# Performance work log

Hardware: AMD Instinct MI355X
Metric: run time of the kernel (lower is better)

## Reference

```python
import jax, jax.numpy as jnp
import numpy as np

# MLA (multi-head latent attention) config
DIM = 1024
HEADS = 16
DIM_HEAD = DIM // HEADS          # 64
LATENT = DIM // 4                # 256, compressed KV latent dim
SCALE = DIM_HEAD ** -0.5


def setup_inputs() -> dict:
    key = jax.random.key(0)
    ks = jax.random.split(key, 8)
    B, S = 2, 2048
    init = lambda k, shape, fan_in: jax.random.normal(k, shape, jnp.float32) * (fan_in ** -0.5)
    return {
        "x":  jax.random.normal(ks[0], (B, S, DIM), jnp.float32),
        "Wq": init(ks[1], (DIM, DIM), DIM),
        "bq": jnp.zeros((DIM,), jnp.float32),
        "Wl": init(ks[2], (DIM, LATENT), DIM),      # down-projection to compressed KV latent
        "bl": jnp.zeros((LATENT,), jnp.float32),
        "Wk": init(ks[3], (LATENT, DIM), LATENT),   # latent -> per-head keys
        "bk": jnp.zeros((DIM,), jnp.float32),
        "Wv": init(ks[4], (LATENT, DIM), LATENT),   # latent -> per-head values
        "bv": jnp.zeros((DIM,), jnp.float32),
        "Wo": init(ks[5], (DIM, DIM), DIM),         # Attention.to_out
        "bo": jnp.zeros((DIM,), jnp.float32),
    }


def reference(x, Wq, bq, Wl, bl, Wk, bk, Wv, bv, Wo, bo):
    B, S, D = x.shape
    H, Dh = HEADS, DIM_HEAD
    # query projection
    q = (x @ Wq + bq).reshape(B, S, H, Dh)
    # compressed KV latent (this is what would be cached; kv_cache=None here)
    latent = x @ Wl + bl                              # [B, S, LATENT]
    k = (latent @ Wk + bk).reshape(B, S, H, Dh)
    v = (latent @ Wv + bv).reshape(B, S, H, Dh)
    # attention
    scores = jnp.einsum('bihd,bjhd->bhij', q, k) * SCALE   # [B, H, S, S]
    attn = jax.nn.softmax(scores, axis=-1)
    out = jnp.einsum('bhij,bjhd->bihd', attn, v).reshape(B, S, D)
    # dropout(p=0) is identity; output projection
    out = out @ Wo + bo
    return out
```

## Files before the change

kernel.cpp:

```cpp
#include <hip/hip_runtime.h>


typedef _Float16 half8  __attribute__((ext_vector_type(8)));
typedef _Float16 half4  __attribute__((ext_vector_type(4)));
typedef float    floatx4 __attribute__((ext_vector_type(4)));

__global__ __launch_bounds__(256) void prep(
    const float* __restrict__ x,
    const float* __restrict__ Wq, const float* __restrict__ Wl,
    const float* __restrict__ Wk, const float* __restrict__ Wv,
    const float* __restrict__ Wo,
    _Float16* __restrict__ xh,
    _Float16* __restrict__ Bt1, _Float16* __restrict__ Bt2,
    _Float16* __restrict__ Wot)
{
    const int t = threadIdx.x;
    if (blockIdx.z == 5) {
        size_t base = ((size_t)(blockIdx.y * 32 + blockIdx.x) * 256 + t) * 16;
#pragma unroll
        for (int it = 0; it < 4; ++it) {
            floatx4 v = *(const floatx4*)(x + base + it * 4);
            *(half4*)(xh + base + it * 4) = __builtin_convertvector(v, half4);
        }
        return;
    }
    const float* src; _Float16* dst; int K, N;
    switch (blockIdx.z) {
        case 0:  src = Wq; dst = Bt1;                 K = 1024; N = 1024; break;
        case 1:  src = Wl; dst = Bt1 + 1024 * 1024;   K = 1024; N = 256;  break;
        case 2:  src = Wk; dst = Bt2;                 K = 256;  N = 1024; break;
        case 3:  src = Wv; dst = Bt2 + 1024 * 256;    K = 256;  N = 1024; break;
        default: src = Wo; dst = Wot;                 K = 1024; N = 1024; break;
    }
    const int n0 = blockIdx.x * 32, k0 = blockIdx.y * 32;
    if (n0 >= N || k0 >= K) return;
    __shared__ _Float16 tile[32][33];
    const int tx = t & 31, ty = t >> 5;
#pragma unroll
    for (int i = 0; i < 4; ++i)
        tile[ty + 8 * i][tx] = (_Float16)src[(size_t)(k0 + ty + 8 * i) * N + n0 + tx];
    __syncthreads();
#pragma unroll
    for (int i = 0; i < 4; ++i)
        dst[(size_t)(n0 + ty + 8 * i) * K + k0 + tx] = tile[tx][ty + 8 * i];
}

template <int MODE>
__global__ __launch_bounds__(256) void gemm_fused(
    const _Float16* __restrict__ A, const _Float16* __restrict__ Bt,
    const float* __restrict__ bias0, const float* __restrict__ bias1,
    void* __restrict__ out0, void* __restrict__ out1,
    int N, int K)
{
    __shared__ _Float16 As[128 * 64];
    __shared__ _Float16 Bs[64 * 64];
    __shared__ _Float16 Tt[(MODE == 1) ? 64 * 136 : 1];
    const int t = threadIdx.x;
    const int lane = t & 63, w = t >> 6;
    const int quad = lane >> 4, low = lane & 15;
    const int row0 = blockIdx.y * 128, col0 = blockIdx.x * 64;
    const int wm = (w >> 1) * 64, wn = (w & 1) * 32;

    floatx4 acc[4][2];
    const floatx4 z4 = {0.f, 0.f, 0.f, 0.f};
#pragma unroll
    for (int i = 0; i < 4; ++i)
#pragma unroll
        for (int j = 0; j < 2; ++j) acc[i][j] = z4;

    const int srow8 = lane >> 3;
    const int sslot = lane & 7;
    const int fswz = (low & 7);

    for (int k0 = 0; k0 < K; k0 += 64) {
        __syncthreads();
#pragma unroll
        for (int c = 0; c < 4; ++c) {
            const int chunk = w * 4 + c;
            const int row = chunk * 8 + srow8;
            const int g = sslot ^ (row & 7);
            const _Float16* gp = A + (size_t)(row0 + row) * K + k0 + g * 8;
            __builtin_amdgcn_global_load_lds(
                (const __attribute__((address_space(1))) void*)gp,
                (__attribute__((address_space(3))) void*)(As + chunk * 512), 16, 0, 0);
        }
#pragma unroll
        for (int c = 0; c < 2; ++c) {
            const int chunk = w * 2 + c;
            const int row = chunk * 8 + srow8;
            const int g = sslot ^ (row & 7);
            const _Float16* gp = Bt + (size_t)(col0 + row) * K + k0 + g * 8;
            __builtin_amdgcn_global_load_lds(
                (const __attribute__((address_space(1))) void*)gp,
                (__attribute__((address_space(3))) void*)(Bs + chunk * 512), 16, 0, 0);
        }
        __syncthreads();

#pragma unroll
        for (int kk = 0; kk < 2; ++kk) {
            const int slot = ((4 * kk + quad) ^ fswz) << 3;
            half8 a[4], b[2];
#pragma unroll
            for (int i = 0; i < 4; ++i)
                a[i] = *(const half8*)(As + (wm + i * 16 + low) * 64 + slot);
#pragma unroll
            for (int j = 0; j < 2; ++j)
                b[j] = *(const half8*)(Bs + (wn + j * 16 + low) * 64 + slot);
#pragma unroll
            for (int i = 0; i < 4; ++i)
#pragma unroll
                for (int j = 0; j < 2; ++j)
                    acc[i][j] = __builtin_amdgcn_mfma_f32_16x16x32_f16(a[i], b[j], acc[i][j], 0, 0, 0);
        }
    }

    if (MODE == 1 && col0 >= 1024) {
        const int hh = (col0 - 1024) >> 6;
        const int bb = row0 >> 11;
        const int tok0 = row0 & 2047;
#pragma unroll
        for (int i = 0; i < 4; ++i)
#pragma unroll
            for (int j = 0; j < 2; ++j) {
                const int lc = wn + j * 16 + low;
                float bv = bias1[hh * 64 + lc];
                half4 ph;
#pragma unroll
                for (int r = 0; r < 4; ++r) ph[r] = (_Float16)(acc[i][j][r] + bv);
                *(half4*)(&Tt[lc * 136 + wm + i * 16 + quad * 4]) = ph;
            }
        __syncthreads();
        _Float16* vb = (_Float16*)out1 + ((size_t)(bb * 16 + hh) * 64) * 2048;
#pragma unroll
        for (int it = 0; it < 4; ++it) {
            const int e = t + 256 * it;
            const int d = e >> 4, tk = (e & 15) * 8;
            half8 val = *(const half8*)(&Tt[d * 136 + tk]);
            *(half8*)(vb + (size_t)d * 2048 + tok0 + tk) = val;
        }
        return;
    }

#pragma unroll
    for (int i = 0; i < 4; ++i) {
#pragma unroll
        for (int j = 0; j < 2; ++j) {
            const int col = col0 + wn + j * 16 + low;
            const int rbase = row0 + wm + i * 16 + quad * 4;
            if (MODE == 2) {
                const float bv = bias0[col];
#pragma unroll
                for (int r = 0; r < 4; ++r)
                    ((float*)out0)[(size_t)(rbase + r) * 1024 + col] = acc[i][j][r] + bv;
            } else if (col < 1024) {
                float bv = bias0[col];
#pragma unroll
                for (int r = 0; r < 4; ++r) {
                    float val = acc[i][j][r] + bv;
                    if (MODE == 0) val *= 0.125f;
                    ((_Float16*)out0)[(size_t)(rbase + r) * 1024 + col] = (_Float16)val;
                }
            } else {
                const int c2 = col - 1024;
                float bv = bias1[c2];
#pragma unroll
                for (int r = 0; r < 4; ++r)
                    ((_Float16*)out1)[(size_t)(rbase + r) * 256 + c2] =
                        (_Float16)(acc[i][j][r] + bv);
            }
        }
    }
}

__global__ __launch_bounds__(256, 4) void mla_attn(
    const _Float16* __restrict__ qp,
    const _Float16* __restrict__ kk,
    const _Float16* __restrict__ vt,
    _Float16* __restrict__ Op0, _Float16* __restrict__ Op1,
    float* __restrict__ lp)
{
    constexpr int S = 2048;
    __shared__ _Float16 Ks[64][76];
    __shared__ _Float16 Vs[64][76];
    __shared__ _Float16 Ps[128][76];

    const int t = threadIdx.x, lane = t & 63, w = t >> 6;
    const int quad = lane >> 4, low = lane & 15;
    const int q0 = blockIdx.x * 128;
    const int b = blockIdx.y >> 4, h = blockIdx.y & 15;
    const int split = blockIdx.z;

    half8 qf[2][2];
#pragma unroll
    for (int ni = 0; ni < 2; ++ni)
#pragma unroll
        for (int ks = 0; ks < 2; ++ks)
            qf[ni][ks] = *(const half8*)(qp +
                (size_t)(b * S + q0 + w * 32 + ni * 16 + low) * 1024 +
                h * 64 + ks * 32 + quad * 8);

    floatx4 oa[2][4], ls[2];
    const floatx4 z4 = {0.f, 0.f, 0.f, 0.f};
#pragma unroll
    for (int mi = 0; mi < 2; ++mi) {
        ls[mi] = z4;
#pragma unroll
        for (int nd = 0; nd < 4; ++nd) oa[mi][nd] = z4;
    }

    const _Float16* kbase = kk + (size_t)(b * S) * 1024 + h * 64;
    const _Float16* vbase = vt + (size_t)(b * 16 + h) * 64 * 2048;

    const int jbeg = split * 1024, jend = jbeg + 1024;
    for (int j0 = jbeg; j0 < jend; j0 += 64) {
        __syncthreads();
#pragma unroll
        for (int p = 0; p < 2; ++p) {
            int c = p * 256 + t;
            int r = c >> 3, o8 = (c & 7) * 8;
            *(half8*)(&Ks[r][o8]) = *(const half8*)(kbase + (size_t)(j0 + r) * 1024 + o8);
            *(half8*)(&Vs[r][o8]) = *(const half8*)(vbase + (size_t)r * 2048 + j0 + o8);
        }
        __syncthreads();

        floatx4 s[4][2];
        const floatx4 i4 = {-3.f, -3.f, -3.f, -3.f};
#pragma unroll
        for (int mj = 0; mj < 4; ++mj)
#pragma unroll
            for (int ni = 0; ni < 2; ++ni) s[mj][ni] = i4;
#pragma unroll
        for (int ks = 0; ks < 2; ++ks) {
            half8 af[4];
#pragma unroll
            for (int mj = 0; mj < 4; ++mj)
                af[mj] = *(const half8*)(&Ks[mj * 16 + low][ks * 32 + quad * 8]);
#pragma unroll
            for (int mj = 0; mj < 4; ++mj)
#pragma unroll
                for (int ni = 0; ni < 2; ++ni)
                    s[mj][ni] = __builtin_amdgcn_mfma_f32_16x16x32_f16(af[mj], qf[ni][ks], s[mj][ni], 0, 0, 0);
        }

#pragma unroll
        for (int mj = 0; mj < 4; ++mj)
#pragma unroll
            for (int ni = 0; ni < 2; ++ni) {
                floatx4 pv;
#pragma unroll
                for (int r = 0; r < 4; ++r) pv[r] = __expf(s[mj][ni][r]);
                ls[ni] += pv;
                half4 ph;
#pragma unroll
                for (int r = 0; r < 4; ++r) ph[r] = (_Float16)pv[r];
                *(half4*)(&Ps[w * 32 + ni * 16 + low][mj * 16 + quad * 4]) = ph;
            }

#pragma unroll
        for (int ks = 0; ks < 2; ++ks) {
            half8 pf[2], vf[4];
#pragma unroll
            for (int mi = 0; mi < 2; ++mi)
                pf[mi] = *(const half8*)(&Ps[w * 32 + mi * 16 + low][ks * 32 + quad * 8]);
#pragma unroll
            for (int nd = 0; nd < 4; ++nd)
                vf[nd] = *(const half8*)(&Vs[nd * 16 + low][ks * 32 + quad * 8]);
#pragma unroll
            for (int mi = 0; mi < 2; ++mi)
#pragma unroll
                for (int nd = 0; nd < 4; ++nd)
                    oa[mi][nd] = __builtin_amdgcn_mfma_f32_16x16x32_f16(pf[mi], vf[nd], oa[mi][nd], 0, 0, 0);
        }
    }

#pragma unroll
    for (int ni = 0; ni < 2; ++ni) {
        float l = ls[ni][0] + ls[ni][1] + ls[ni][2] + ls[ni][3];
        l += __shfl_xor(l, 16);
        l += __shfl_xor(l, 32);
        if (quad == 0)
            lp[split * 65536 + (b * 16 + h) * 2048 + q0 + w * 32 + ni * 16 + low] = l;
    }
    _Float16* op = split ? Op1 : Op0;
#pragma unroll
    for (int mi = 0; mi < 2; ++mi)
#pragma unroll
        for (int nd = 0; nd < 4; ++nd)
#pragma unroll
            for (int r = 0; r < 4; ++r)
                op[(size_t)(b * S + q0 + w * 32 + mi * 16 + quad * 4 + r) * 1024 +
                   h * 64 + nd * 16 + low] = (_Float16)oa[mi][nd][r];
}

__global__ __launch_bounds__(256) void attn_combine(
    const _Float16* __restrict__ O0, const _Float16* __restrict__ O1,
    const float* __restrict__ lp, _Float16* __restrict__ att)
{
    size_t idx = ((size_t)blockIdx.x * 256 + threadIdx.x) * 8;
    int row = (int)(idx >> 10), c = (int)(idx & 1023);
    int b = row >> 11, qq = row & 2047, h = c >> 6;
    int li = (b * 16 + h) * 2048 + qq;
    float inv = 1.f / (lp[li] + lp[65536 + li]);
    half8 a = *(const half8*)(O0 + idx);
    half8 bb = *(const half8*)(O1 + idx);
    half8 o;
#pragma unroll
    for (int r = 0; r < 8; ++r)
        o[r] = (_Float16)(((float)a[r] + (float)bb[r]) * inv);
    *(half8*)(att + idx) = o;
}

extern "C" void kernel_launch(void* const* d_in, const int* in_sizes, int n_in,
                              void* d_out, int out_size, void* d_ws, size_t ws_size,
                              hipStream_t stream) {
    const float* x  = (const float*)d_in[0];
    const float* Wq = (const float*)d_in[1];
    const float* bq = (const float*)d_in[2];
    const float* Wl = (const float*)d_in[3];
    const float* bl = (const float*)d_in[4];
    const float* Wk = (const float*)d_in[5];
    const float* bk = (const float*)d_in[6];
    const float* Wv = (const float*)d_in[7];
    const float* bv = (const float*)d_in[8];
    const float* Wo = (const float*)d_in[9];
    const float* bo = (const float*)d_in[10];
    float* out = (float*)d_out;

    _Float16* p   = (_Float16*)d_ws;
    _Float16* xh  = p; p += 4194304;
    _Float16* qh  = p; p += 4194304;
    _Float16* kh  = p; p += 4194304;
    _Float16* vtb = p; p += 4194304;
    _Float16* ah  = p; p += 4194304;
    _Float16* lat = p; p += 1048576;
    _Float16* Bt1 = p; p += 1310720;
    _Float16* Bt2 = p; p += 524288;
    _Float16* Wot = p; p += 1048576;

    prep<<<dim3(32, 32, 6), 256, 0, stream>>>(x, Wq, Wl, Wk, Wv, Wo, xh, Bt1, Bt2, Wot);

    gemm_fused<0><<<dim3(20, 32), 256, 0, stream>>>(
        xh, Bt1, bq, bl, qh, lat, 1280, 1024);
    gemm_fused<1><<<dim3(32, 32), 256, 0, stream>>>(
        lat, Bt2, bk, bv, kh, vtb, 2048, 256);
    mla_attn<<<dim3(16, 32, 2), 256, 0, stream>>>(qh, kh, vtb, ah, xh, (float*)lat);
    attn_combine<<<2048, 256, 0, stream>>>(ah, xh, (const float*)lat, kh);
    gemm_fused<2><<<dim3(16, 32), 256, 0, stream>>>(
        kh, Wot, bo, nullptr, out, nullptr, 1024, 1024);
}
```

Before: 211.7 us.

## Keep P in registers via 32x32 MFMA and permlane swap, swizzle K/V LDS

Rewrites the attention inner loop to use 32x32x16 MFMA tiles so the exponentiated score tile can be repacked into the A operand of the PV matmul with v_permlane32_swap instead of staging P through shared memory. The padded K/V/P shared buffers become unpadded K/V tiles with an XOR-and-rotate swizzle to avoid bank conflicts. The P buffer and its LDS round-trip are removed and the occupancy hint on launch bounds is dropped. In exchange the fragment layout mapping is more intricate and register pressure per wave changes.

```diff
diff --git a/kernel.cpp b/kernel.cpp
--- a/kernel.cpp
+++ b/kernel.cpp
@@ -4,6 +4,7 @@
 typedef _Float16 half8  __attribute__((ext_vector_type(8)));
 typedef _Float16 half4  __attribute__((ext_vector_type(4)));
 typedef float    floatx4 __attribute__((ext_vector_type(4)));
+typedef float    floatx16 __attribute__((ext_vector_type(16)));
 
 __global__ __launch_bounds__(256) void prep(
     const float* __restrict__ x,
@@ -172,7 +173,12 @@
     }
 }
 
-__global__ __launch_bounds__(256, 4) void mla_attn(
+__device__ __forceinline__ unsigned pk2(float a, float b) {
+    union { _Float16 h[2]; unsigned u; } x;
+    x.h[0] = (_Float16)a; x.h[1] = (_Float16)b; return x.u;
+}
+
+__global__ __launch_bounds__(256) void mla_attn(
     const _Float16* __restrict__ qp,
     const _Float16* __restrict__ kk,
     const _Float16* __restrict__ vt,
@@ -180,33 +186,28 @@
     float* __restrict__ lp)
 {
     constexpr int S = 2048;
-    __shared__ _Float16 Ks[64][76];
-    __shared__ _Float16 Vs[64][76];
-    __shared__ _Float16 Ps[128][76];
+    __shared__ _Float16 Ks[64 * 64];
+    __shared__ _Float16 Vs[64 * 64];
 
     const int t = threadIdx.x, lane = t & 63, w = t >> 6;
-    const int quad = lane >> 4, low = lane & 15;
+    const int l31 = lane & 31, hi = lane >> 5;
+    const int rho = l31 & 7, sig = l31 >> 3;
     const int q0 = blockIdx.x * 128;
     const int b = blockIdx.y >> 4, h = blockIdx.y & 15;
     const int split = blockIdx.z;
 
-    half8 qf[2][2];
-#pragma unroll
-    for (int ni = 0; ni < 2; ++ni)
-#pragma unroll
-        for (int ks = 0; ks < 2; ++ks)
-            qf[ni][ks] = *(const half8*)(qp +
-                (size_t)(b * S + q0 + w * 32 + ni * 16 + low) * 1024 +
-                h * 64 + ks * 32 + quad * 8);
-
-    floatx4 oa[2][4], ls[2];
-    const floatx4 z4 = {0.f, 0.f, 0.f, 0.f};
-#pragma unroll
-    for (int mi = 0; mi < 2; ++mi) {
-        ls[mi] = z4;
-#pragma unroll
-        for (int nd = 0; nd < 4; ++nd) oa[mi][nd] = z4;
-    }
+    half8 qf[4];
+#pragma unroll
+    for (int ks = 0; ks < 4; ++ks)
+        qf[ks] = *(const half8*)(qp +
+            (size_t)(b * S + q0 + w * 32 + l31) * 1024 + h * 64 + ks * 16 + hi * 8);
+
+    floatx16 oa[2];
+#pragma unroll
+    for (int nd = 0; nd < 2; ++nd)
+#pragma unroll
+        for (int r = 0; r < 16; ++r) oa[nd][r] = 0.f;
+    float ls = 0.f;
 
     const _Float16* kbase = kk + (size_t)(b * S) * 1024 + h * 64;
     const _Float16* vbase = vt + (size_t)(b * 16 + h) * 64 * 2048;
@@ -216,80 +217,81 @@
         __syncthreads();
 #pragma unroll
         for (int p = 0; p < 2; ++p) {
-            int c = p * 256 + t;
-            int r = c >> 3, o8 = (c & 7) * 8;
-            *(half8*)(&Ks[r][o8]) = *(const half8*)(kbase + (size_t)(j0 + r) * 1024 + o8);
-            *(half8*)(&Vs[r][o8]) = *(const half8*)(vbase + (size_t)r * 2048 + j0 + o8);
-        }
-        __syncthreads();
-
-        floatx4 s[4][2];
-        const floatx4 i4 = {-3.f, -3.f, -3.f, -3.f};
-#pragma unroll
-        for (int mj = 0; mj < 4; ++mj)
-#pragma unroll
-            for (int ni = 0; ni < 2; ++ni) s[mj][ni] = i4;
-#pragma unroll
-        for (int ks = 0; ks < 2; ++ks) {
-            half8 af[4];
-#pragma unroll
-            for (int mj = 0; mj < 4; ++mj)
-                af[mj] = *(const half8*)(&Ks[mj * 16 + low][ks * 32 + quad * 8]);
-#pragma unroll
-            for (int mj = 0; mj < 4; ++mj)
-#pragma unroll
-                for (int ni = 0; ni < 2; ++ni)
-                    s[mj][ni] = __builtin_amdgcn_mfma_f32_16x16x32_f16(af[mj], qf[ni][ks], s[mj][ni], 0, 0, 0);
-        }
-
-#pragma unroll
-        for (int mj = 0; mj < 4; ++mj)
-#pragma unroll
-            for (int ni = 0; ni < 2; ++ni) {
-                floatx4 pv;
-#pragma unroll
-                for (int r = 0; r < 4; ++r) pv[r] = __expf(s[mj][ni][r]);
-                ls[ni] += pv;
-                half4 ph;
-#pragma unroll
-                for (int r = 0; r < 4; ++r) ph[r] = (_Float16)pv[r];
-                *(half4*)(&Ps[w * 32 + ni * 16 + low][mj * 16 + quad * 4]) = ph;
-            }
-
-#pragma unroll
-        for (int ks = 0; ks < 2; ++ks) {
-            half8 pf[2], vf[4];
-#pragma unroll
-            for (int mi = 0; mi < 2; ++mi)
-                pf[mi] = *(const half8*)(&Ps[w * 32 + mi * 16 + low][ks * 32 + quad * 8]);
-#pragma unroll
-            for (int nd = 0; nd < 4; ++nd)
-                vf[nd] = *(const half8*)(&Vs[nd * 16 + low][ks * 32 + quad * 8]);
-#pragma unroll
-            for (int mi = 0; mi < 2; ++mi)
-#pragma unroll
-                for (int nd = 0; nd < 4; ++nd)
-                    oa[mi][nd] = __builtin_amdgcn_mfma_f32_16x16x32_f16(pf[mi], vf[nd], oa[mi][nd], 0, 0, 0);
-        }
-    }
-
-#pragma unroll
-    for (int ni = 0; ni < 2; ++ni) {
-        float l = ls[ni][0] + ls[ni][1] + ls[ni][2] + ls[ni][3];
-        l += __shfl_xor(l, 16);
-        l += __shfl_xor(l, 32);
-        if (quad == 0)
-            lp[split * 65536 + (b * 16 + h) * 2048 + q0 + w * 32 + ni * 16 + low] = l;
-    }
+            const int c = p * 256 + t;
+            const int r = c >> 3, g = c & 7;
+            const int s8 = ((g ^ (r & 7)) + (r >> 3)) & 7;
+            *(half8*)(Ks + r * 64 + s8 * 8) =
+                *(const half8*)(kbase + (size_t)(j0 + r) * 1024 + g * 8);
+            *(half8*)(Vs + r * 64 + s8 * 8) =
+                *(const half8*)(vbase + (size_t)r * 2048 + j0 + g * 8);
+        }
+        __syncthreads();
+
+        floatx16 sc[2];
+#pragma unroll
+        for (int jb = 0; jb < 2; ++jb)
+#pragma unroll
+            for (int r = 0; r < 16; ++r) sc[jb][r] = -3.f;
+
+#pragma unroll
+        for (int jb = 0; jb < 2; ++jb)
+#pragma unroll
+            for (int ks = 0; ks < 4; ++ks) {
+                const int row = jb * 32 + l31;
+                const int s8 = (((2 * ks + hi) ^ rho) + sig + 4 * jb) & 7;
+                half8 kf = *(const half8*)(Ks + row * 64 + s8 * 8);
+                sc[jb] = __builtin_amdgcn_mfma_f32_32x32x16_f16(kf, qf[ks], sc[jb], 0, 0, 0);
+            }
+
+        half8 pfrag[2][2];
+#pragma unroll
+        for (int jb = 0; jb < 2; ++jb) {
+#pragma unroll
+            for (int r = 0; r < 16; ++r) {
+                sc[jb][r] = __expf(sc[jb][r]);
+                ls += sc[jb][r];
+            }
+#pragma unroll
+            for (int kb = 0; kb < 2; ++kb) {
+                unsigned a0 = pk2(sc[jb][8 * kb + 0], sc[jb][8 * kb + 1]);
+                unsigned a1 = pk2(sc[jb][8 * kb + 2], sc[jb][8 * kb + 3]);
+                unsigned b0 = pk2(sc[jb][8 * kb + 4], sc[jb][8 * kb + 5]);
+                unsigned b1 = pk2(sc[jb][8 * kb + 6], sc[jb][8 * kb + 7]);
+                asm("v_permlane32_swap_b32 %0, %1" : "+v"(a0), "+v"(b0));
+                asm("v_permlane32_swap_b32 %0, %1" : "+v"(a1), "+v"(b1));
+                union { unsigned u[4]; half8 h; } pu;
+                pu.u[0] = a0; pu.u[1] = a1; pu.u[2] = b0; pu.u[3] = b1;
+                pfrag[jb][kb] = pu.h;
+            }
+        }
+
+#pragma unroll
+        for (int jb = 0; jb < 2; ++jb)
+#pragma unroll
+            for (int kb = 0; kb < 2; ++kb)
+#pragma unroll
+                for (int nd = 0; nd < 2; ++nd) {
+                    const int row = nd * 32 + l31;
+                    const int g = 4 * jb + 2 * kb + hi;
+                    const int s8 = ((g ^ rho) + sig + 4 * nd) & 7;
+                    half8 vf = *(const half8*)(Vs + row * 64 + s8 * 8);
+                    oa[nd] = __builtin_amdgcn_mfma_f32_32x32x16_f16(pfrag[jb][kb], vf, oa[nd], 0, 0, 0);
+                }
+    }
+
+    float l2 = ls + __shfl_xor(ls, 32);
+    if (hi == 0)
+        lp[split * 65536 + (b * 16 + h) * 2048 + q0 + w * 32 + l31] = l2;
+
     _Float16* op = split ? Op1 : Op0;
 #pragma unroll
-    for (int mi = 0; mi < 2; ++mi)
-#pragma unroll
-        for (int nd = 0; nd < 4; ++nd)
-#pragma unroll
-            for (int r = 0; r < 4; ++r)
-                op[(size_t)(b * S + q0 + w * 32 + mi * 16 + quad * 4 + r) * 1024 +
-                   h * 64 + nd * 16 + low] = (_Float16)oa[mi][nd][r];
+    for (int nd = 0; nd < 2; ++nd)
+#pragma unroll
+        for (int r = 0; r < 16; ++r) {
+            const int qrow = (r & 3) + 8 * (r >> 2) + 4 * hi;
+            op[(size_t)(b * S + q0 + w * 32 + qrow) * 1024 +
+               h * 64 + nd * 32 + l31] = (_Float16)oa[nd][r];
+        }
 }
 
 __global__ __launch_bounds__(256) void attn_combine(
```

Measured after the change: 206.0 us. -2.7%, faster.
